# Performance work log

Hardware: AMD Instinct MI355X
Metric: run time of the kernel (lower is better)

The kernel has to match this reference:

```python
import jax, jax.numpy as jnp
import numpy as np

EPS = 1e-5

def _branch(x, W, gamma, beta):
    # 1x1 conv (no bias) + InstanceNorm2d(affine) + ReLU
    y = jnp.einsum('oc,bchw->bohw', W, x)
    mu = y.mean(axis=(2, 3), keepdims=True)
    var = y.var(axis=(2, 3), keepdims=True)
    y = (y - mu) * jax.lax.rsqrt(var + EPS)
    y = y * gamma[None, :, None, None] + beta[None, :, None, None]
    return jax.nn.relu(y)

def setup_inputs() -> dict:
    key = jax.random.key(0)
    ks = jax.random.split(key, 12)
    b, in_ch, h, w = 2, 256, 64, 64
    c = in_ch // 8
    d = dict(
        x1=jax.random.normal(ks[0], (b, in_ch, h, w), jnp.float32),
        x2=jax.random.normal(ks[1], (b, in_ch, h, w), jnp.float32),
        x3=jax.random.normal(ks[2], (b, in_ch, h, w), jnp.float32),
        W1=jax.random.normal(ks[3], (c, in_ch), jnp.float32) * (1.0 / np.sqrt(in_ch)),
        g1=jnp.ones((c,), jnp.float32), b1=jnp.zeros((c,), jnp.float32),
        W2=jax.random.normal(ks[4], (c, in_ch), jnp.float32) * (1.0 / np.sqrt(in_ch)),
        g2=jnp.ones((c,), jnp.float32), b2=jnp.zeros((c,), jnp.float32),
        W3=jax.random.normal(ks[5], (c, in_ch), jnp.float32) * (1.0 / np.sqrt(in_ch)),
        g3=jnp.ones((c,), jnp.float32), b3=jnp.zeros((c,), jnp.float32),
    )
    return d

def _forward(x1, x2, x3, W1, g1, b1, W2, g2, b2, W3, g3, b3):
    q1 = _branch(x1, W1, g1, b1); q2 = _branch(x2, W1, g1, b1); q3 = _branch(x3, W1, g1, b1)
    k1 = _branch(x1, W2, g2, b2); k2 = _branch(x2, W2, g2, b2); k3 = _branch(x3, W2, g2, b2)
    v1 = _branch(x1, W3, g3, b3); v2 = _branch(x2, W3, g3, b3); v3 = _branch(x3, W3, g3, b3)
    b_, c, h, w = q1.shape
    hw = h * w
    Q1 = q1.reshape(b_, c, hw).transpose(0, 2, 1)  # [b,hw,c]
    Q2 = q2.reshape(b_, c, hw).transpose(0, 2, 1)
    Q3 = q3.reshape(b_, c, hw).transpose(0, 2, 1)
    K1 = k1.reshape(b_, c, hw)                      # [b,c,hw]
    K2 = k2.reshape(b_, c, hw)
    K3 = k3.reshape(b_, c, hw)
    sm = lambda Q, K: jax.nn.softmax(jnp.einsum('bic,bcj->bij', Q, K), axis=-1)
    A12 = sm(Q1, K2); A21 = sm(Q2, K1); A23 = sm(Q2, K3)
    A32 = sm(Q3, K2); A13 = sm(Q1, K3)
    # ones[b,c,hw] @ A == broadcast of column-sums of A: track a [b,hw] vector
    colsum = lambda A: A.sum(axis=1)                        # [b,hw]
    step = lambda v, A: jnp.einsum('bk,bkj->bj', v, A)      # [b,hw]
    def bc(v):  # broadcast [b,hw] -> [b,c,h,w]
        return jnp.broadcast_to(v[:, None, :], (b_, c, hw)).reshape(b_, c, h, w)
    p1a = bc(step(step(step(colsum(A12), A23), A32), A21))
    p1b = bc(step(colsum(A12), A21))
    p2 = bc(step(colsum(A23), A32))
    p3a = bc(step(colsum(A12), A23))
    p3b = bc(colsum(A13))
    return (p1a, p1b, p2, p3a, p3b, v1, v2, v3)

def reference(x1, x2, x3, W1, g1, b1, W2, g2, b2, W3, g3, b3):
    return _forward(x1, x2, x3, W1, g1, b1, W2, g2, b2, W3, g3, b3)
```

## Files before the change

### kernel.cpp

```cpp
#include <hip/hip_runtime.h>

typedef unsigned short u16;
typedef u16  u16x8  __attribute__((ext_vector_type(8)));
typedef _Float16 f16x4 __attribute__((ext_vector_type(4)));
typedef _Float16 f16x8 __attribute__((ext_vector_type(8)));
typedef float f32x2 __attribute__((ext_vector_type(2)));
typedef float f32x4 __attribute__((ext_vector_type(4)));

#define HW 4096
#define CIN 256
#define HW32 (HW * 32)
#define L2E 1.4426950408889634f

__device__ __forceinline__ float fexp2(float x) { return __builtin_amdgcn_exp2f(x); }

__global__ __launch_bounds__(256) void convert_kernel(const float* x1, const float* x2, const float* x3,
        const float* W1, const float* W2, const float* W3,
        _Float16* xh, _Float16* wh, float* mean, float* maxq, float* maxk) {
    int bx = blockIdx.x; int t = threadIdx.x;
    if (bx < 1536) {
        int xi = bx >> 9, b = (bx >> 8) & 1, c = bx & 255;
        const float* src = (xi == 0 ? x1 : xi == 1 ? x2 : x3) + (size_t)(b * CIN + c) * HW;
        _Float16* dst = xh + ((size_t)((xi * 2 + b) * CIN) + c) * HW;
        float s = 0.f;
        for (int i = t; i < 1024; i += 256) {
            f32x4 v = ((const f32x4*)src)[i];
            s += v[0] + v[1] + v[2] + v[3];
            f16x4 h;
#pragma unroll
            for (int r = 0; r < 4; ++r) h[r] = (_Float16)v[r];
            ((f16x4*)dst)[i] = h;
        }
        __shared__ float red[256];
        red[t] = s; __syncthreads();
        for (int k = 128; k; k >>= 1) { if (t < k) red[t] += red[t + k]; __syncthreads(); }
        if (t == 0) mean[(xi * 2 + b) * CIN + c] = red[0] * (1.f / HW);
    } else {
        int j = bx - 1536;
        if (j == 0 && t < 12) { if (t < 6) maxq[t] = 0.f; else maxk[t - 6] = 0.f; }
        int widx = j >> 1, half = j & 1;
        const float* wsrc = (widx == 0 ? W1 : widx == 1 ? W2 : W3) + half * 4096;
        _Float16* wdst = wh + widx * 8192 + half * 4096;
        for (int i = t; i < 1024; i += 256) {
            f32x4 v = ((const f32x4*)wsrc)[i];
            f16x4 h;
#pragma unroll
            for (int r = 0; r < 4; ++r) h[r] = (_Float16)v[r];
            ((f16x4*)wdst)[i] = h;
        }
    }
}

__global__ __launch_bounds__(256) void m2_kernel(const _Float16* xh, float* Pm2) {
    int xi = blockIdx.y, b = blockIdx.z;
    int xb = xi * 2 + b;
    const _Float16* X = xh + (size_t)xb * CIN * HW;
    int bx = blockIdx.x;
    int chunk = bx >> 4, blk = bx & 15;
    int t = threadIdx.x; int wv = t >> 6; int L = t & 63; int m = L & 15; int quad = L >> 4;
    int region = blk * 4 + wv;
    int r1 = (region >> 3) * 32, r2 = (region & 7) * 32;
    int p0 = chunk * 512 + quad * 8;
    const f16x8* A0 = (const f16x8*)(X + (size_t)(r1 + m) * HW + p0);
    const f16x8* A1 = (const f16x8*)(X + (size_t)(r1 + 16 + m) * HW + p0);
    const f16x8* B0 = (const f16x8*)(X + (size_t)(r2 + m) * HW + p0);
    const f16x8* B1 = (const f16x8*)(X + (size_t)(r2 + 16 + m) * HW + p0);
    f32x4 zero = {0, 0, 0, 0};
    f32x4 acc00 = zero, acc01 = zero, acc10 = zero, acc11 = zero;
#pragma unroll 4
    for (int it = 0; it < 16; ++it) {
        f16x8 a0 = A0[it * 4], a1 = A1[it * 4];
        f16x8 b0 = B0[it * 4], b1 = B1[it * 4];
        acc00 = __builtin_amdgcn_mfma_f32_16x16x32_f16(a0, b0, acc00, 0, 0, 0);
        acc01 = __builtin_amdgcn_mfma_f32_16x16x32_f16(a0, b1, acc01, 0, 0, 0);
        acc10 = __builtin_amdgcn_mfma_f32_16x16x32_f16(a1, b0, acc10, 0, 0, 0);
        acc11 = __builtin_amdgcn_mfma_f32_16x16x32_f16(a1, b1, acc11, 0, 0, 0);
    }
    float* dst = Pm2 + ((size_t)chunk * 6 + xb) * 65536;
#pragma unroll
    for (int r = 0; r < 4; ++r) {
        int row0 = (r1 + quad * 4 + r) * 256, row1 = (r1 + 16 + quad * 4 + r) * 256;
        dst[row0 + r2 + m] = acc00[r];
        dst[row0 + r2 + 16 + m] = acc01[r];
        dst[row1 + r2 + m] = acc10[r];
        dst[row1 + r2 + 16 + m] = acc11[r];
    }
}

__global__ __launch_bounds__(256) void m2combine_kernel(const float* Pm2, float* M2) {
    size_t e = (size_t)blockIdx.x * 256 + threadIdx.x;
    float s = 0.f;
#pragma unroll
    for (int c = 0; c < 8; ++c) s += Pm2[(size_t)c * 6 * 65536 + e];
    M2[e] = s * (1.f / HW);
}

__global__ __launch_bounds__(256) void stats_kernel(const float* M2, const float* mean,
        const float* W1, const float* W2, const float* W3,
        const float* g1, const float* g2, const float* g3,
        const float* b1, const float* b2, const float* b3, float2* afine) {
    int o = blockIdx.x; int xi = blockIdx.y; int b = blockIdx.z;
    int widx = o >> 5; int oc = o & 31;
    const float* Wp = (widx == 0 ? W1 : widx == 1 ? W2 : W3) + oc * CIN;
    const float* gp = (widx == 0 ? g1 : widx == 1 ? g2 : g3);
    const float* bp = (widx == 0 ? b1 : widx == 1 ? b2 : b3);
    int t = threadIdx.x;
    __shared__ float sW[256];
    __shared__ float red[256];
    sW[t] = Wp[t];
    __syncthreads();
    const float* m2row = M2 + ((size_t)(xi * 2 + b) * CIN + t) * CIN;
    float tv = 0.f;
    const f32x4* r4 = (const f32x4*)m2row;
#pragma unroll 4
    for (int k = 0; k < 64; ++k) {
        f32x4 mv = r4[k];
        const f32x4 wv = *(const f32x4*)&sW[k * 4];
        tv += mv[0] * wv[0] + mv[1] * wv[1] + mv[2] * wv[2] + mv[3] * wv[3];
    }
    red[t] = tv * sW[t]; __syncthreads();
    for (int k = 128; k; k >>= 1) { if (t < k) red[t] += red[t + k]; __syncthreads(); }
    float E2 = red[0]; __syncthreads();
    red[t] = sW[t] * mean[(xi * 2 + b) * CIN + t]; __syncthreads();
    for (int k = 128; k; k >>= 1) { if (t < k) red[t] += red[t + k]; __syncthreads(); }
    if (t == 0) {
        float mu = red[0];
        float var = E2 - mu * mu;
        float rsig = rsqrtf(var + 1e-5f);
        float scale = gp[oc] * rsig;
        float bias = bp[oc] - mu * scale;
        if (widx == 0) { scale *= L2E; bias *= L2E; }
        afine[(xi * 2 + b) * 96 + o] = make_float2(scale, bias);
    }
}

__global__ __launch_bounds__(256) void conv_kernel(const _Float16* xh, const _Float16* wh,
        const float2* afine, _Float16* qT, _Float16* kT, float* out,
        float* maxq, float* maxk) {
    int xi = blockIdx.y, b = blockIdx.z;
    const u16* xb = (const u16*)(xh + (size_t)(xi * 2 + b) * CIN * HW);
    int p0 = blockIdx.x * 64;
    __shared__ u16 lds[32 * 65 * 8];
    __shared__ float smq[4], smk[4];
    int t = threadIdx.x;
    {
        int pc = t & 7, cg = t >> 3;
        u16x8 a[8];
#pragma unroll
        for (int r = 0; r < 8; ++r)
            a[r] = *(const u16x8*)(xb + (size_t)(cg * 8 + r) * HW + p0 + pc * 8);
#pragma unroll
        for (int i = 0; i < 8; ++i) {
            u16x8 d;
#pragma unroll
            for (int r = 0; r < 8; ++r) d[r] = a[r][i];
            int p = pc * 8 + i; int fp = p ^ (p >> 3);
            *(u16x8*)&lds[(cg * 65 + fp) * 8] = d;
        }
    }
    __syncthreads();
    int wv = t >> 6, L = t & 63, m = L & 15, quad = L >> 4;
    int pw0 = wv * 16;
    f16x8 af[8];
    {
        int p = pw0 + m; int fp = p ^ (p >> 3);
#pragma unroll
        for (int k = 0; k < 8; ++k)
            af[k] = *(const f16x8*)&lds[((k * 4 + quad) * 65 + fp) * 8];
    }
    int xb2 = xi * 2 + b;
    float sqq[4] = {0, 0, 0, 0}, sqk[4] = {0, 0, 0, 0};
    for (int ot = 0; ot < 6; ++ot) {
        int o0 = ot * 16; int widx = ot >> 1;
        int o_col = o0 + m;
        f32x4 acc = {0, 0, 0, 0};
#pragma unroll
        for (int k = 0; k < 8; ++k) {
            f16x8 bfr = *(const f16x8*)(wh + (size_t)o_col * CIN + k * 32 + quad * 8);
            acc = __builtin_amdgcn_mfma_f32_16x16x32_f16(af[k], bfr, acc, 0, 0, 0);
        }
        float2 afv = afine[xb2 * 96 + o_col];
        f32x4 vals;
#pragma unroll
        for (int r = 0; r < 4; ++r) {
            float v = acc[r] * afv.x + afv.y;
            vals[r] = v > 0.f ? v : 0.f;
        }
        int prow = p0 + pw0 + quad * 4;
        if (widx < 2) {
            _Float16* dst = (widx == 0 ? qT : kT) + (size_t)xb2 * HW32;
            int cc = (o0 & 31) + m;
#pragma unroll
            for (int r = 0; r < 4; ++r)
                dst[(size_t)(prow + r) * 32 + cc] = (_Float16)vals[r];
            if (widx == 0) {
#pragma unroll
                for (int r = 0; r < 4; ++r) sqq[r] += vals[r] * vals[r];
            } else {
#pragma unroll
                for (int r = 0; r < 4; ++r) sqk[r] += vals[r] * vals[r];
            }
        } else {
            float* dst = out + (size_t)(5 + xi) * 262144 + (size_t)b * 131072 + (size_t)(o_col - 64) * HW + prow;
            *(f32x4*)dst = vals;
        }
    }
#pragma unroll
    for (int msk = 1; msk <= 8; msk <<= 1) {
#pragma unroll
        for (int r = 0; r < 4; ++r) {
            sqq[r] += __shfl_xor(sqq[r], msk);
            sqk[r] += __shfl_xor(sqk[r], msk);
        }
    }
    float nq = fmaxf(fmaxf(sqq[0], sqq[1]), fmaxf(sqq[2], sqq[3]));
    float nk = fmaxf(fmaxf(sqk[0], sqk[1]), fmaxf(sqk[2], sqk[3]));
    nq = fmaxf(nq, __shfl_xor(nq, 16)); nq = fmaxf(nq, __shfl_xor(nq, 32));
    nk = fmaxf(nk, __shfl_xor(nk, 16)); nk = fmaxf(nk, __shfl_xor(nk, 32));
    if (L == 0) { smq[wv] = nq; smk[wv] = nk; }
    __syncthreads();
    if (t == 0) {
        float bq = fmaxf(fmaxf(smq[0], smq[1]), fmaxf(smq[2], smq[3]));
        float bk = fmaxf(fmaxf(smk[0], smk[1]), fmaxf(smk[2], smk[3]));
        atomicMax((unsigned*)&maxq[xb2], __float_as_uint(bq));
        atomicMax((unsigned*)&maxk[xb2], __float_as_uint(bk));
    }
}

__global__ __launch_bounds__(256) void zsweep_kernel(const _Float16* qT, const _Float16* kT,
        const float* maxq, const float* maxk, float* Pz) {
    const int qxA[5] = {0, 1, 1, 2, 0};
    const int kxA[5] = {1, 0, 2, 1, 2};
    int mat = blockIdx.y, b = blockIdx.z;
    const _Float16* qb = qT + (size_t)(qxA[mat] * 2 + b) * HW32;
    const _Float16* kb = kT + (size_t)(kxA[mat] * 2 + b) * HW32;
    float Cg = sqrtf(maxq[qxA[mat] * 2 + b]) * sqrtf(maxk[kxA[mat] * 2 + b]);
    int bx = blockIdx.x;
    int jc = bx & 7, qblk = bx >> 3;
    int t = threadIdx.x; int wv = t >> 6; int L = t & 63; int m = L & 15; int quad = L >> 4;
    int i0 = qblk * 256 + wv * 64;
    f16x8 a[4];
#pragma unroll
    for (int tt = 0; tt < 4; ++tt)
        a[tt] = *(const f16x8*)(qb + (size_t)(i0 + tt * 16 + m) * 32 + quad * 8);
    const f16x8* kp = (const f16x8*)(kb + m * 32 + quad * 8) + (size_t)jc * (32 * 64);
    f32x4 negC = {-Cg, -Cg, -Cg, -Cg};
    f32x4 zero = {0.f, 0.f, 0.f, 0.f};
    f32x4 z[4] = {zero, zero, zero, zero};
#pragma unroll 4
    for (int j = 0; j < 32; ++j) {
        f16x8 bf = kp[j * 64];
#pragma unroll
        for (int tt = 0; tt < 4; ++tt) {
            f32x4 d = __builtin_amdgcn_mfma_f32_16x16x32_f16(a[tt], bf, negC, 0, 0, 0);
            f32x4 e = {fexp2(d[0]), fexp2(d[1]), fexp2(d[2]), fexp2(d[3])};
            z[tt] = z[tt] + e;
        }
    }
#pragma unroll
    for (int tt = 0; tt < 4; ++tt)
#pragma unroll
        for (int msk = 1; msk <= 8; msk <<= 1) {
            z[tt][0] += __shfl_xor(z[tt][0], msk); z[tt][1] += __shfl_xor(z[tt][1], msk);
            z[tt][2] += __shfl_xor(z[tt][2], msk); z[tt][3] += __shfl_xor(z[tt][3], msk);
        }
    if (m == 0) {
        int mb = mat * 2 + b;
#pragma unroll
        for (int tt = 0; tt < 4; ++tt) {
            int row = i0 + tt * 16 + quad * 4;
#pragma unroll
            for (int r = 0; r < 4; ++r)
                Pz[((size_t)mb * 8 + jc) * HW + row + r] = z[tt][r];
        }
    }
}

struct PCfg {
    const _Float16* qb; const _Float16* kb;
    const float* mq; const float* mk;
    const float* PzR;
    const float2* w1src;
    const float2* w2src;
    float2* Pp;
    int nit;
    int ic1, comp1, ic2, comp2;
};

__global__ __launch_bounds__(256) void pass2p_kernel(PCfg c0, PCfg c1) {
    PCfg c = (blockIdx.y == 0) ? c0 : c1;
    int b = blockIdx.z;
    int bx = blockIdx.x; int jb = bx & 15; int ic = bx >> 4;
    const _Float16* qb = c.qb + (size_t)b * HW32;
    const _Float16* kb = c.kb + (size_t)b * HW32;
    float Cg = sqrtf(c.mq[b]) * sqrtf(c.mk[b]);
    int t = threadIdx.x; int wv = t >> 6; int L = t & 63; int m = L & 15; int quad = L >> 4;
    int ibase = ic * (c.nit * 16);
    int rows = c.nit * 16;
    __shared__ float2 wlds[256];
    {
        for (int r = t; r < rows; r += 256) {
            int i = ibase + r;
            const float* pz = c.PzR + (size_t)b * (8 * HW) + i;
            float Z = 0.f;
#pragma unroll
            for (int cc = 0; cc < 8; ++cc) Z += pz[cc * HW];
            float rz = 1.0f / Z;
            float wx, wy = 0.f;
            if (c.w1src) {
                float s = 0.f;
                for (int cc = 0; cc < c.ic1; ++cc) {
                    float2 p = c.w1src[((size_t)cc * 2 + b) * HW + i];
                    s += c.comp1 ? p.y : p.x;
                }
                wx = s * rz;
            } else wx = rz;
            if (c.w2src) {
                float s = 0.f;
                for (int cc = 0; cc < c.ic2; ++cc) {
                    float2 p = c.w2src[((size_t)cc * 2 + b) * HW + i];
                    s += c.comp2 ? p.y : p.x;
                }
                wy = s * rz;
            }
            wlds[r] = make_float2(wx, wy);
        }
    }
    __syncthreads();
    int j0 = jb * 256 + wv * 64;
    f16x8 bf[4];
#pragma unroll
    for (int tt = 0; tt < 4; ++tt)
        bf[tt] = *(const f16x8*)(kb + (size_t)(j0 + tt * 16 + m) * 32 + quad * 8);
    f32x4 negC = {-Cg, -Cg, -Cg, -Cg};
    f32x2 acc[4] = {{0, 0}, {0, 0}, {0, 0}, {0, 0}};
    int dual = (c.w2src != nullptr);
    if (dual) {
#pragma unroll 4
        for (int it = 0; it < c.nit; ++it) {
            int i0 = ibase + it * 16;
            f16x8 av = *(const f16x8*)(qb + (size_t)(i0 + m) * 32 + quad * 8);
            const float2* wr = &wlds[it * 16 + quad * 4];
            f32x2 w0 = {wr[0].x, wr[0].y}, w1 = {wr[1].x, wr[1].y};
            f32x2 w2 = {wr[2].x, wr[2].y}, w3 = {wr[3].x, wr[3].y};
#pragma unroll
            for (int tt = 0; tt < 4; ++tt) {
                f32x4 d = __builtin_amdgcn_mfma_f32_16x16x32_f16(av, bf[tt], negC, 0, 0, 0);
                float e0 = fexp2(d[0]), e1 = fexp2(d[1]), e2 = fexp2(d[2]), e3 = fexp2(d[3]);
                acc[tt] += (f32x2){e0, e0} * w0;
                acc[tt] += (f32x2){e1, e1} * w1;
                acc[tt] += (f32x2){e2, e2} * w2;
                acc[tt] += (f32x2){e3, e3} * w3;
            }
        }
    } else {
#pragma unroll 4
        for (int it = 0; it < c.nit; ++it) {
            int i0 = ibase + it * 16;
            f16x8 av = *(const f16x8*)(qb + (size_t)(i0 + m) * 32 + quad * 8);
            const float2* wr = &wlds[it * 16 + quad * 4];
            float w0 = wr[0].x, w1 = wr[1].x, w2 = wr[2].x, w3 = wr[3].x;
#pragma unroll
            for (int tt = 0; tt < 4; ++tt) {
                f32x4 d = __builtin_amdgcn_mfma_f32_16x16x32_f16(av, bf[tt], negC, 0, 0, 0);
                float e0 = fexp2(d[0]), e1 = fexp2(d[1]), e2 = fexp2(d[2]), e3 = fexp2(d[3]);
                acc[tt][0] += e0 * w0 + e1 * w1 + e2 * w2 + e3 * w3;
            }
        }
    }
#pragma unroll
    for (int tt = 0; tt < 4; ++tt) {
        acc[tt][0] += __shfl_xor(acc[tt][0], 16); acc[tt][0] += __shfl_xor(acc[tt][0], 32);
        acc[tt][1] += __shfl_xor(acc[tt][1], 16); acc[tt][1] += __shfl_xor(acc[tt][1], 32);
    }
    if (quad == 0) {
        float2* dst = c.Pp + ((size_t)ic * 2 + b) * HW;
#pragma unroll
        for (int tt = 0; tt < 4; ++tt)
            dst[j0 + tt * 16 + m] = make_float2(acc[tt][0], acc[tt][1]);
    }
}

__global__ __launch_bounds__(256) void bcast_kernel(const float2* PpA2, const float2* PpB,
        const float2* PpC, const float2* PpD, float* out) {
    int bx = blockIdx.x;
    int sb = bx >> 4; int s = sb >> 1; int b = sb & 1; int js = bx & 15;
    int j = js * 256 + threadIdx.x;
    float v = 0.f;
    if (s == 0)      { for (int ic = 0; ic < 32; ++ic) v += PpD[((size_t)ic * 2 + b) * HW + j].x; }
    else if (s == 1) { for (int ic = 0; ic < 32; ++ic) v += PpD[((size_t)ic * 2 + b) * HW + j].y; }
    else if (s == 2) { for (int ic = 0; ic < 32; ++ic) v += PpC[((size_t)ic * 2 + b) * HW + j].x; }
    else if (s == 3) { for (int ic = 0; ic < 32; ++ic) v += PpB[((size_t)ic * 2 + b) * HW + j].y; }
    else             { for (int ic = 0; ic < 16; ++ic) v += PpA2[((size_t)ic * 2 + b) * HW + j].x; }
    float* dst = out + ((size_t)(s * 2 + b) * 32) * HW + j;
#pragma unroll
    for (int c = 0; c < 32; ++c) dst[(size_t)c * HW] = v;
}

extern "C" void kernel_launch(void* const* d_in, const int* in_sizes, int n_in,
                              void* d_out, int out_size, void* d_ws, size_t ws_size,
                              hipStream_t stream) {
    (void)in_sizes; (void)n_in; (void)out_size; (void)ws_size;
    const float* x1 = (const float*)d_in[0];
    const float* x2 = (const float*)d_in[1];
    const float* x3 = (const float*)d_in[2];
    const float* W1 = (const float*)d_in[3];
    const float* g1 = (const float*)d_in[4];
    const float* b1 = (const float*)d_in[5];
    const float* W2 = (const float*)d_in[6];
    const float* g2 = (const float*)d_in[7];
    const float* b2 = (const float*)d_in[8];
    const float* W3 = (const float*)d_in[9];
    const float* g3 = (const float*)d_in[10];
    const float* b3 = (const float*)d_in[11];
    float* out = (float*)d_out;

    char* w = (char*)d_ws;
    _Float16* xh    = (_Float16*)(w);
    _Float16* wh    = (_Float16*)(w + 12582912);
    float*    mean  = (float*)(w + 12632064);
    float*    M2    = (float*)(w + 12638208);
    float2*   afine = (float2*)(w + 14211072);
    _Float16* qT    = (_Float16*)(w + 14215680);
    _Float16* kT    = (_Float16*)(w + 15788544);
    float*    maxq  = (float*)(w + 17525248);
    float*    maxk  = (float*)(w + 17525312);
    float*    Pz    = (float*)(w + 18213376);
    float2*   PpA   = (float2*)(w + 23456256);
    float2*   PpB   = (float2*)(w + 25553408);
    float2*   PpC   = (float2*)(w + 27650560);
    float2*   PpD   = (float2*)(w + 29747712);
    float*    Pm2   = (float*)(w + 18213376);
    float2*   PpA2  = PpA + 16 * 2 * HW;

    hipLaunchKernelGGL(convert_kernel, dim3(1542), dim3(256), 0, stream,
                       x1, x2, x3, W1, W2, W3, xh, wh, mean, maxq, maxk);
    hipLaunchKernelGGL(m2_kernel, dim3(128, 3, 2), dim3(256), 0, stream, xh, Pm2);
    hipLaunchKernelGGL(m2combine_kernel, dim3(1536), dim3(256), 0, stream, Pm2, M2);
    hipLaunchKernelGGL(stats_kernel, dim3(96, 3, 2), dim3(256), 0, stream,
                       M2, mean, W1, W2, W3, g1, g2, g3, b1, b2, b3, afine);
    hipLaunchKernelGGL(conv_kernel, dim3(64, 3, 2), dim3(256), 0, stream,
                       xh, wh, afine, qT, kT, out, maxq, maxk);
    hipLaunchKernelGGL(zsweep_kernel, dim3(128, 5, 2), dim3(256), 0, stream, qT, kT, maxq, maxk, Pz);

    PCfg cA0 = { qT + 0 * 2 * HW32, kT + 1 * 2 * HW32, maxq + 0, maxk + 2,
                 Pz + (size_t)0 * 16 * HW, nullptr, nullptr, PpA,  16, 0, 0, 0, 0 };
    PCfg cA1 = { qT + 0 * 2 * HW32, kT + 2 * 2 * HW32, maxq + 0, maxk + 4,
                 Pz + (size_t)4 * 16 * HW, nullptr, nullptr, PpA2, 16, 0, 0, 0, 0 };
    hipLaunchKernelGGL(pass2p_kernel, dim3(256, 2, 2), dim3(256), 0, stream, cA0, cA1);

    PCfg cB = { qT + 1 * 2 * HW32, kT + 2 * 2 * HW32, maxq + 2, maxk + 4,
                Pz + (size_t)2 * 16 * HW, nullptr, PpA, PpB, 8, 0, 0, 16, 0 };
    hipLaunchKernelGGL(pass2p_kernel, dim3(512, 1, 2), dim3(256), 0, stream, cB, cB);

    PCfg cC = { qT + 2 * 2 * HW32, kT + 1 * 2 * HW32, maxq + 4, maxk + 2,
                Pz + (size_t)3 * 16 * HW, PpB, PpB, PpC, 8, 32, 0, 32, 1 };
    hipLaunchKernelGGL(pass2p_kernel, dim3(512, 1, 2), dim3(256), 0, stream, cC, cC);

    PCfg cD = { qT + 1 * 2 * HW32, kT + 0 * 2 * HW32, maxq + 2, maxk + 0,
                Pz + (size_t)1 * 16 * HW, PpC, PpA, PpD, 8, 32, 1, 16, 0 };
    hipLaunchKernelGGL(pass2p_kernel, dim3(512, 1, 2), dim3(256), 0, stream, cD, cD);

    hipLaunchKernelGGL(bcast_kernel, dim3(160), dim3(256), 0, stream, PpA2, PpB, PpC, PpD, out);
}
```

Measured before the change: 263.4 us.

## Split stats into strip-parallel partial and finalize kernels, widen conv grid

```diff
diff --git a/kernel.cpp b/kernel.cpp
--- a/kernel.cpp
+++ b/kernel.cpp
@@ -16,7 +16,7 @@
 
 __global__ __launch_bounds__(256) void convert_kernel(const float* x1, const float* x2, const float* x3,
         const float* W1, const float* W2, const float* W3,
-        _Float16* xh, _Float16* wh, float* mean, float* maxq, float* maxk) {
+        _Float16* xh, _Float16* wh, float* mean, float* maxq, float* maxk, float* E2buf) {
     int bx = blockIdx.x; int t = threadIdx.x;
     if (bx < 1536) {
         int xi = bx >> 9, b = (bx >> 8) & 1, c = bx & 255;
@@ -37,7 +37,10 @@
         if (t == 0) mean[(xi * 2 + b) * CIN + c] = red[0] * (1.f / HW);
     } else {
         int j = bx - 1536;
-        if (j == 0 && t < 12) { if (t < 6) maxq[t] = 0.f; else maxk[t - 6] = 0.f; }
+        if (j == 0) {
+            if (t < 12) { if (t < 6) maxq[t] = 0.f; else maxk[t - 6] = 0.f; }
+            for (int i = t; i < 576; i += 256) E2buf[i] = 0.f;
+        }
         int widx = j >> 1, half = j & 1;
         const float* wsrc = (widx == 0 ? W1 : widx == 1 ? W2 : W3) + half * 4096;
         _Float16* wdst = wh + widx * 8192 + half * 4096;
@@ -95,43 +98,56 @@
     M2[e] = s * (1.f / HW);
 }
 
-__global__ __launch_bounds__(256) void stats_kernel(const float* M2, const float* mean,
+__global__ __launch_bounds__(256) void stats_part(const float* M2,
+        const float* W1, const float* W2, const float* W3, float* E2buf) {
+    int strip = blockIdx.x;
+    int xi = blockIdx.y, b = blockIdx.z; int xb = xi * 2 + b;
+    __shared__ float rowM[4][256];
+    int t = threadIdx.x;
+    const float* m2b = M2 + ((size_t)xb * 256 + strip * 4) * 256;
+    for (int i = t; i < 1024; i += 256) rowM[i >> 8][i & 255] = m2b[i];
+    __syncthreads();
+    for (int task = t; task < 384; task += 256) {
+        int o = task % 96; int c1 = task / 96;
+        int widx = o >> 5, oc = o & 31;
+        const float* Wp = (widx == 0 ? W1 : widx == 1 ? W2 : W3) + oc * 256;
+        const f32x4* wr4 = (const f32x4*)Wp;
+        const f32x4* mr4 = (const f32x4*)rowM[c1];
+        float dot = 0.f;
+#pragma unroll 4
+        for (int k = 0; k < 64; ++k) {
+            f32x4 a = mr4[k], wv = wr4[k];
+            dot += a[0] * wv[0] + a[1] * wv[1] + a[2] * wv[2] + a[3] * wv[3];
+        }
+        atomicAdd(&E2buf[xb * 96 + o], dot * Wp[strip * 4 + c1]);
+    }
+}
+
+__global__ __launch_bounds__(96) void stats_fin(const float* E2buf, const float* mean,
         const float* W1, const float* W2, const float* W3,
         const float* g1, const float* g2, const float* g3,
         const float* b1, const float* b2, const float* b3, float2* afine) {
-    int o = blockIdx.x; int xi = blockIdx.y; int b = blockIdx.z;
-    int widx = o >> 5; int oc = o & 31;
-    const float* Wp = (widx == 0 ? W1 : widx == 1 ? W2 : W3) + oc * CIN;
+    int o = threadIdx.x;
+    int xi = blockIdx.x, b = blockIdx.y; int xb = xi * 2 + b;
+    int widx = o >> 5, oc = o & 31;
+    const float* Wp = (widx == 0 ? W1 : widx == 1 ? W2 : W3) + oc * 256;
     const float* gp = (widx == 0 ? g1 : widx == 1 ? g2 : g3);
     const float* bp = (widx == 0 ? b1 : widx == 1 ? b2 : b3);
-    int t = threadIdx.x;
-    __shared__ float sW[256];
-    __shared__ float red[256];
-    sW[t] = Wp[t];
-    __syncthreads();
-    const float* m2row = M2 + ((size_t)(xi * 2 + b) * CIN + t) * CIN;
-    float tv = 0.f;
-    const f32x4* r4 = (const f32x4*)m2row;
+    const float* mn = mean + xb * CIN;
+    float mu = 0.f;
+    const f32x4* w4 = (const f32x4*)Wp; const f32x4* m4 = (const f32x4*)mn;
 #pragma unroll 4
     for (int k = 0; k < 64; ++k) {
-        f32x4 mv = r4[k];
-        const f32x4 wv = *(const f32x4*)&sW[k * 4];
-        tv += mv[0] * wv[0] + mv[1] * wv[1] + mv[2] * wv[2] + mv[3] * wv[3];
-    }
-    red[t] = tv * sW[t]; __syncthreads();
-    for (int k = 128; k; k >>= 1) { if (t < k) red[t] += red[t + k]; __syncthreads(); }
-    float E2 = red[0]; __syncthreads();
-    red[t] = sW[t] * mean[(xi * 2 + b) * CIN + t]; __syncthreads();
-    for (int k = 128; k; k >>= 1) { if (t < k) red[t] += red[t + k]; __syncthreads(); }
-    if (t == 0) {
-        float mu = red[0];
-        float var = E2 - mu * mu;
-        float rsig = rsqrtf(var + 1e-5f);
-        float scale = gp[oc] * rsig;
-        float bias = bp[oc] - mu * scale;
-        if (widx == 0) { scale *= L2E; bias *= L2E; }
-        afine[(xi * 2 + b) * 96 + o] = make_float2(scale, bias);
-    }
+        f32x4 wv = w4[k], mv = m4[k];
+        mu += wv[0] * mv[0] + wv[1] * mv[1] + wv[2] * mv[2] + wv[3] * mv[3];
+    }
+    float E2 = E2buf[xb * 96 + o];
+    float var = E2 - mu * mu;
+    float rsig = rsqrtf(var + 1e-5f);
+    float scale = gp[oc] * rsig;
+    float bias = bp[oc] - mu * scale;
+    if (widx == 0) { scale *= L2E; bias *= L2E; }
+    afine[xb * 96 + o] = make_float2(scale, bias);
 }
 
 __global__ __launch_bounds__(256) void conv_kernel(const _Float16* xh, const _Float16* wh,
@@ -139,9 +155,11 @@
         float* maxq, float* maxk) {
     int xi = blockIdx.y, b = blockIdx.z;
     const u16* xb = (const u16*)(xh + (size_t)(xi * 2 + b) * CIN * HW);
-    int p0 = blockIdx.x * 64;
+    int bxx = blockIdx.x;
+    int pair = bxx >> 6;
+    int p0 = (bxx & 63) * 64;
     __shared__ u16 lds[32 * 65 * 8];
-    __shared__ float smq[4], smk[4];
+    __shared__ float sm[4];
     int t = threadIdx.x;
     {
         int pc = t & 7, cg = t >> 3;
@@ -169,9 +187,11 @@
             af[k] = *(const f16x8*)&lds[((k * 4 + quad) * 65 + fp) * 8];
     }
     int xb2 = xi * 2 + b;
-    float sqq[4] = {0, 0, 0, 0}, sqk[4] = {0, 0, 0, 0};
-    for (int ot = 0; ot < 6; ++ot) {
-        int o0 = ot * 16; int widx = ot >> 1;
+    float sq[4] = {0, 0, 0, 0};
+#pragma unroll
+    for (int oi = 0; oi < 2; ++oi) {
+        int ot = pair * 2 + oi;
+        int o0 = ot * 16;
         int o_col = o0 + m;
         f32x4 acc = {0, 0, 0, 0};
 #pragma unroll
@@ -187,43 +207,33 @@
             vals[r] = v > 0.f ? v : 0.f;
         }
         int prow = p0 + pw0 + quad * 4;
-        if (widx < 2) {
-            _Float16* dst = (widx == 0 ? qT : kT) + (size_t)xb2 * HW32;
+        if (pair < 2) {
+            _Float16* dst = (pair == 0 ? qT : kT) + (size_t)xb2 * HW32;
             int cc = (o0 & 31) + m;
 #pragma unroll
             for (int r = 0; r < 4; ++r)
                 dst[(size_t)(prow + r) * 32 + cc] = (_Float16)vals[r];
-            if (widx == 0) {
-#pragma unroll
-                for (int r = 0; r < 4; ++r) sqq[r] += vals[r] * vals[r];
-            } else {
-#pragma unroll
-                for (int r = 0; r < 4; ++r) sqk[r] += vals[r] * vals[r];
-            }
+#pragma unroll
+            for (int r = 0; r < 4; ++r) sq[r] += vals[r] * vals[r];
         } else {
             float* dst = out + (size_t)(5 + xi) * 262144 + (size_t)b * 131072 + (size_t)(o_col - 64) * HW + prow;
             *(f32x4*)dst = vals;
         }
     }
-#pragma unroll
-    for (int msk = 1; msk <= 8; msk <<= 1) {
-#pragma unroll
-        for (int r = 0; r < 4; ++r) {
-            sqq[r] += __shfl_xor(sqq[r], msk);
-            sqk[r] += __shfl_xor(sqk[r], msk);
-        }
-    }
-    float nq = fmaxf(fmaxf(sqq[0], sqq[1]), fmaxf(sqq[2], sqq[3]));
-    float nk = fmaxf(fmaxf(sqk[0], sqk[1]), fmaxf(sqk[2], sqk[3]));
-    nq = fmaxf(nq, __shfl_xor(nq, 16)); nq = fmaxf(nq, __shfl_xor(nq, 32));
-    nk = fmaxf(nk, __shfl_xor(nk, 16)); nk = fmaxf(nk, __shfl_xor(nk, 32));
-    if (L == 0) { smq[wv] = nq; smk[wv] = nk; }
-    __syncthreads();
-    if (t == 0) {
-        float bq = fmaxf(fmaxf(smq[0], smq[1]), fmaxf(smq[2], smq[3]));
-        float bk = fmaxf(fmaxf(smk[0], smk[1]), fmaxf(smk[2], smk[3]));
-        atomicMax((unsigned*)&maxq[xb2], __float_as_uint(bq));
-        atomicMax((unsigned*)&maxk[xb2], __float_as_uint(bk));
+    if (pair < 2) {
+#pragma unroll
+        for (int msk = 1; msk <= 8; msk <<= 1) {
+#pragma unroll
+            for (int r = 0; r < 4; ++r) sq[r] += __shfl_xor(sq[r], msk);
+        }
+        float n = fmaxf(fmaxf(sq[0], sq[1]), fmaxf(sq[2], sq[3]));
+        n = fmaxf(n, __shfl_xor(n, 16)); n = fmaxf(n, __shfl_xor(n, 32));
+        if (L == 0) sm[wv] = n;
+        __syncthreads();
+        if (t == 0) {
+            float bn = fmaxf(fmaxf(sm[0], sm[1]), fmaxf(sm[2], sm[3]));
+            atomicMax((unsigned*)(pair == 0 ? &maxq[xb2] : &maxk[xb2]), __float_as_uint(bn));
+        }
     }
 }
 
@@ -425,6 +435,7 @@
     _Float16* kT    = (_Float16*)(w + 15788544);
     float*    maxq  = (float*)(w + 17525248);
     float*    maxk  = (float*)(w + 17525312);
+    float*    E2buf = (float*)(w + 17525376);
     float*    Pz    = (float*)(w + 18213376);
     float2*   PpA   = (float2*)(w + 23456256);
     float2*   PpB   = (float2*)(w + 25553408);
@@ -434,12 +445,14 @@
     float2*   PpA2  = PpA + 16 * 2 * HW;
 
     hipLaunchKernelGGL(convert_kernel, dim3(1542), dim3(256), 0, stream,
-                       x1, x2, x3, W1, W2, W3, xh, wh, mean, maxq, maxk);
+                       x1, x2, x3, W1, W2, W3, xh, wh, mean, maxq, maxk, E2buf);
     hipLaunchKernelGGL(m2_kernel, dim3(128, 3, 2), dim3(256), 0, stream, xh, Pm2);
     hipLaunchKernelGGL(m2combine_kernel, dim3(1536), dim3(256), 0, stream, Pm2, M2);
-    hipLaunchKernelGGL(stats_kernel, dim3(96, 3, 2), dim3(256), 0, stream,
-                       M2, mean, W1, W2, W3, g1, g2, g3, b1, b2, b3, afine);
-    hipLaunchKernelGGL(conv_kernel, dim3(64, 3, 2), dim3(256), 0, stream,
+    hipLaunchKernelGGL(stats_part, dim3(64, 3, 2), dim3(256), 0, stream,
+                       M2, W1, W2, W3, E2buf);
+    hipLaunchKernelGGL(stats_fin, dim3(3, 2), dim3(96), 0, stream,
+                       E2buf, mean, W1, W2, W3, g1, g2, g3, b1, b2, b3, afine);
+    hipLaunchKernelGGL(conv_kernel, dim3(192, 3, 2), dim3(256), 0, stream,
                        xh, wh, afine, qT, kT, out, maxq, maxk);
     hipLaunchKernelGGL(zsweep_kernel, dim3(128, 5, 2), dim3(256), 0, stream, qT, kT, maxq, maxk, Pz);
 
```

Result: slower. 274.2 us (+4.1%).
